# Kernel tuning notes

Measured on AMD Instinct MI355X. Metric: run time of the kernel, lower is better.

Reference implementation:

```python
import jax, jax.numpy as jnp
import numpy as np

N_NODES = 20000
N_EDGES = 320000
BERT_H = 768
GIN_H = 256
N_LAYERS = 3
EPS = 0.0  # gin_epsilon


def setup_inputs() -> dict:
    key = jax.random.key(0)
    ks = jax.random.split(key, 12)
    node_embed = jax.random.normal(ks[0], (N_NODES, BERT_H), dtype=jnp.float32)
    edge_weight = jax.random.uniform(ks[1], (N_EDGES,), dtype=jnp.float32)
    src = jax.random.randint(ks[2], (N_EDGES,), 0, N_NODES, dtype=jnp.int32)
    dst = jax.random.randint(ks[3], (N_EDGES,), 0, N_NODES, dtype=jnp.int32)
    s = 0.02
    W0 = jax.random.normal(ks[4], (BERT_H, GIN_H), dtype=jnp.float32) * s
    b0 = jnp.zeros((GIN_H,), dtype=jnp.float32)
    W1 = jax.random.normal(ks[5], (GIN_H, GIN_H), dtype=jnp.float32) * s
    b1 = jnp.zeros((GIN_H,), dtype=jnp.float32)
    W2 = jax.random.normal(ks[6], (GIN_H, GIN_H), dtype=jnp.float32) * s
    b2 = jnp.zeros((GIN_H,), dtype=jnp.float32)
    Wr = jax.random.normal(ks[7], (N_LAYERS * GIN_H, GIN_H), dtype=jnp.float32) * s
    br = jnp.zeros((GIN_H,), dtype=jnp.float32)
    return {"node_embed": node_embed, "edge_weight": edge_weight,
            "W0": W0, "b0": b0, "W1": W1, "b1": b1, "W2": W2, "b2": b2,
            "Wr": Wr, "br": br, "src": src, "dst": dst}


def _gin_layer(h, edge_weight, src, dst, W, b):
    # edge-weighted sum aggregation: agg_i = sum_{(j->i)} w_ji * h_j
    msgs = h[src] * edge_weight[:, None]          # [E, d]
    agg = jax.ops.segment_sum(msgs, dst, num_segments=N_NODES)  # [N, d]
    rst = (1.0 + EPS) * h + agg
    return jax.nn.relu(rst @ W + b)


def reference(node_embed, edge_weight, W0, b0, W1, b1, W2, b2, Wr, br, src, dst):
    params = [(W0, b0), (W1, b1), (W2, b2)]
    h = node_embed
    outs = []
    for (W, b) in params:
        h = _gin_layer(h, edge_weight, src, dst, W, b)
        outs.append(h)
    cat = jnp.concatenate(outs, axis=-1)          # [N, n_layers*gin_h]
    return jax.nn.relu(cat) @ Wr + br             # [N, gin_h]
```

## Files before the change

kernel.cpp:

```cpp
#include <hip/hip_runtime.h>

#define NN 20000
#define NE 320000
#define BH 768
#define GH 256

typedef __attribute__((ext_vector_type(8))) short short8;
typedef __attribute__((ext_vector_type(4))) float f32x4;

__device__ __forceinline__ ushort f2bf(float x) {
    union { float f; unsigned u; } v; v.f = x;
    unsigned r = (v.u + 0x7FFFu + ((v.u >> 16) & 1u)) >> 16;
    return (ushort)r;
}
__device__ __forceinline__ float bf2f(ushort h) {
    union { unsigned u; float f; } v; v.u = ((unsigned)h) << 16;
    return v.f;
}
__device__ __forceinline__ ushort f2h(float x) {
    union { _Float16 h; ushort u; } v; v.h = (_Float16)x; return v.u;
}
__device__ __forceinline__ float h2f(ushort u) {
    union { _Float16 h; ushort u; } v; v.u = u; return (float)v.h;
}

__device__ __forceinline__ void gload_lds16(const void* g, void* l) {
    __builtin_amdgcn_global_load_lds(
        (const __attribute__((address_space(1))) void*)g,
        (__attribute__((address_space(3))) void*)l, 16, 0, 0);
}


__global__ void k_count(const int* __restrict__ dst, int* __restrict__ cnt, int E) {
    int i = blockIdx.x * blockDim.x + threadIdx.x;
    if (i < E) atomicAdd(&cnt[dst[i]], 1);
}

__global__ __launch_bounds__(1024)
void k_scan(const int* __restrict__ cnt, int* __restrict__ off,
            int* __restrict__ fill, int n) {
    __shared__ int sbuf[1024];
    const int tid  = threadIdx.x;
    const int base = tid * 20;
    int local[20];
    int s = 0;
    #pragma unroll
    for (int i = 0; i < 20; ++i) {
        const int idx = base + i;
        int v = (idx < n) ? cnt[idx] : 0;
        local[i] = s;
        s += v;
    }
    sbuf[tid] = s;
    __syncthreads();
    int sum = s;
    for (int ofs = 1; ofs < 1024; ofs <<= 1) {
        int other = (tid >= ofs) ? sbuf[tid - ofs] : 0;
        __syncthreads();
        sum += other;
        sbuf[tid] = sum;
        __syncthreads();
    }
    const int excl = sum - s;
    #pragma unroll
    for (int i = 0; i < 20; ++i) {
        const int idx = base + i;
        if (idx < n) { const int v = excl + local[i]; off[idx] = v; fill[idx] = v; }
    }
    if (tid == 1023) off[n] = sum;
}

__global__ void k_scatter(const int* __restrict__ src, const int* __restrict__ dst,
                          const float* __restrict__ w, int* __restrict__ fill,
                          int* __restrict__ csr_src, float* __restrict__ csr_w, int E) {
    int i = blockIdx.x * blockDim.x + threadIdx.x;
    if (i < E) {
        int d = dst[i];
        int p = atomicAdd(&fill[d], 1);
        csr_src[p] = src[i];
        csr_w[p]  = w[i];
    }
}


__global__ void k_split(const float* __restrict__ x, ushort* __restrict__ hi,
                        ushort* __restrict__ lo, int n4) {
    int i = blockIdx.x * blockDim.x + threadIdx.x;
    if (i >= n4) return;
    float4 v = ((const float4*)x)[i];
    ushort4 h, l;
    h.x = f2bf(v.x); l.x = f2bf(v.x - bf2f(h.x));
    h.y = f2bf(v.y); l.y = f2bf(v.y - bf2f(h.y));
    h.z = f2bf(v.z); l.z = f2bf(v.z - bf2f(h.z));
    h.w = f2bf(v.w); l.w = f2bf(v.w - bf2f(h.w));
    ((ushort4*)hi)[i] = h;
    ((ushort4*)lo)[i] = l;
}

__global__ void k_splitw(const float* __restrict__ W, ushort* __restrict__ hi,
                         ushort* __restrict__ lo, int K, int N) {
    int id = blockIdx.x * blockDim.x + threadIdx.x;
    if (id >= K * N) return;
    int n = id / K, k = id % K;
    float v = W[(size_t)k * N + n];
    ushort h = f2bf(v);
    hi[id] = h;
    lo[id] = f2bf(v - bf2f(h));
}


__global__ __launch_bounds__(256)
void k_gemm_mfma(const ushort* __restrict__ Ah, const ushort* __restrict__ Al,
                 int lda, int K,
                 const ushort* __restrict__ Bh, const ushort* __restrict__ Bl,
                 const float* __restrict__ bias,
                 float* __restrict__ C, ushort* __restrict__ Ch, int M) {
    __shared__ ushort As_h[2][64 * 32];
    __shared__ ushort As_l[2][64 * 32];
    __shared__ ushort Bs_h[2][128 * 32];
    __shared__ ushort Bs_l[2][128 * 32];

    const int t    = threadIdx.x;
    const int lane = t & 63;
    const int m0   = blockIdx.y * 64;
    const int n0   = blockIdx.x * 128;

    const int ra = t >> 2;
    const int sa = (t & 3) ^ ((ra >> 1) & 3);
    int rga = m0 + ra; if (rga > M - 1) rga = M - 1;
    const size_t aofs = (size_t)rga * lda + (size_t)(sa * 8);
    const int cb1 = t + 256;
    const int rb0 = t >> 2,   rb1 = cb1 >> 2;
    const int sb0 = (t & 3)   ^ ((rb0 >> 1) & 3);
    const int sb1 = (cb1 & 3) ^ ((rb1 >> 1) & 3);
    const size_t bofs0 = (size_t)(n0 + rb0) * K + (size_t)(sb0 * 8);
    const size_t bofs1 = (size_t)(n0 + rb1) * K + (size_t)(sb1 * 8);
    const int d0 = (t >> 6) << 10;
    const int d1 = (cb1 >> 6) << 10;

    const int wm = (t >> 6) & 1;
    const int wn = t >> 7;

    f32x4 zero = (f32x4)0.0f;
    f32x4 acc[2][4];
    #pragma unroll
    for (int i = 0; i < 2; ++i)
        #pragma unroll
        for (int j = 0; j < 4; ++j) acc[i][j] = zero;

    const int fr  = lane & 15;
    const int fsl = lane >> 4;

    auto STAGE = [&](int buf, int k0) {
        gload_lds16(Ah + aofs + k0, (char*)As_h[buf] + d0);
        gload_lds16(Al + aofs + k0, (char*)As_l[buf] + d0);
        gload_lds16(Bh + bofs0 + k0, (char*)Bs_h[buf] + d0);
        gload_lds16(Bh + bofs1 + k0, (char*)Bs_h[buf] + d1);
        gload_lds16(Bl + bofs0 + k0, (char*)Bs_l[buf] + d0);
        gload_lds16(Bl + bofs1 + k0, (char*)Bs_l[buf] + d1);
    };

    STAGE(0, 0);
    int cur = 0;
    for (int k0 = 0; k0 < K; k0 += 32, cur ^= 1) {
        __syncthreads();
        if (k0 + 32 < K) STAGE(cur ^ 1, k0 + 32);

        short8 ah[2], al2[2], bh[4], bl[4];
        #pragma unroll
        for (int i = 0; i < 2; ++i) {
            const int r = wm * 32 + i * 16 + fr;
            const int s = fsl ^ ((r >> 1) & 3);
            ah[i]  = *(const short8*)(&As_h[cur][0] + r * 32 + s * 8);
            al2[i] = *(const short8*)(&As_l[cur][0] + r * 32 + s * 8);
        }
        #pragma unroll
        for (int j = 0; j < 4; ++j) {
            const int r = wn * 64 + j * 16 + fr;
            const int s = fsl ^ ((r >> 1) & 3);
            bh[j] = *(const short8*)(&Bs_h[cur][0] + r * 32 + s * 8);
            bl[j] = *(const short8*)(&Bs_l[cur][0] + r * 32 + s * 8);
        }
        #pragma unroll
        for (int i = 0; i < 2; ++i)
            #pragma unroll
            for (int j = 0; j < 4; ++j) {
                acc[i][j] = __builtin_amdgcn_mfma_f32_16x16x32_bf16(ah[i],  bh[j], acc[i][j], 0, 0, 0);
                acc[i][j] = __builtin_amdgcn_mfma_f32_16x16x32_bf16(ah[i],  bl[j], acc[i][j], 0, 0, 0);
                acc[i][j] = __builtin_amdgcn_mfma_f32_16x16x32_bf16(al2[i], bh[j], acc[i][j], 0, 0, 0);
            }
    }

    #pragma unroll
    for (int i = 0; i < 2; ++i) {
        #pragma unroll
        for (int j = 0; j < 4; ++j) {
            const int col = n0 + wn * 64 + j * 16 + fr;
            const int r0  = m0 + wm * 32 + i * 16 + ((lane >> 4) << 2);
            const float ba = bias ? bias[col] : 0.0f;
            #pragma unroll
            for (int q = 0; q < 4; ++q) {
                const int r = r0 + q;
                if (r < M) {
                    const float v = acc[i][j][q] + ba;
                    C[(size_t)r * 256 + col] = v;
                    if (Ch) Ch[(size_t)r * 256 + col] = f2h(v);
                }
            }
        }
    }
}


__global__ __launch_bounds__(256)
void k_aggregate(const float* __restrict__ y,
                 const ushort* __restrict__ yh,
                 const int* __restrict__ off,
                 const int* __restrict__ csr_src,
                 const float* __restrict__ csr_w,
                 const float* __restrict__ bias,
                 ushort* __restrict__ cat_h,
                 ushort* __restrict__ cat_l,
                 int n) {
    const int wave = blockIdx.x * (blockDim.x >> 6) + (threadIdx.x >> 6);
    const int lane = threadIdx.x & 63;
    if (wave >= n) return;
    const int c = lane * 4;

    float4 self = *(const float4*)(y + (size_t)wave * GH + c);
    float4 b    = *(const float4*)(bias + c);

    float4 a0 = make_float4(0.f, 0.f, 0.f, 0.f);
    float4 a1 = a0, a2 = a0, a3 = a0;
    const int e0 = off[wave], e1 = off[wave + 1];
    int e = e0;
    for (; e + 4 <= e1; e += 4) {
        const int   s0 = csr_src[e],     s1 = csr_src[e + 1];
        const int   s2 = csr_src[e + 2], s3 = csr_src[e + 3];
        const float w0 = csr_w[e],       w1 = csr_w[e + 1];
        const float w2 = csr_w[e + 2],   w3 = csr_w[e + 3];
        ushort4 v0 = *(const ushort4*)(yh + (size_t)s0 * GH + c);
        ushort4 v1 = *(const ushort4*)(yh + (size_t)s1 * GH + c);
        ushort4 v2 = *(const ushort4*)(yh + (size_t)s2 * GH + c);
        ushort4 v3 = *(const ushort4*)(yh + (size_t)s3 * GH + c);
        a0.x = fmaf(w0, h2f(v0.x), a0.x); a0.y = fmaf(w0, h2f(v0.y), a0.y);
        a0.z = fmaf(w0, h2f(v0.z), a0.z); a0.w = fmaf(w0, h2f(v0.w), a0.w);
        a1.x = fmaf(w1, h2f(v1.x), a1.x); a1.y = fmaf(w1, h2f(v1.y), a1.y);
        a1.z = fmaf(w1, h2f(v1.z), a1.z); a1.w = fmaf(w1, h2f(v1.w), a1.w);
        a2.x = fmaf(w2, h2f(v2.x), a2.x); a2.y = fmaf(w2, h2f(v2.y), a2.y);
        a2.z = fmaf(w2, h2f(v2.z), a2.z); a2.w = fmaf(w2, h2f(v2.w), a2.w);
        a3.x = fmaf(w3, h2f(v3.x), a3.x); a3.y = fmaf(w3, h2f(v3.y), a3.y);
        a3.z = fmaf(w3, h2f(v3.z), a3.z); a3.w = fmaf(w3, h2f(v3.w), a3.w);
    }
    for (; e < e1; ++e) {
        const int   s = csr_src[e];
        const float w = csr_w[e];
        ushort4 v = *(const ushort4*)(yh + (size_t)s * GH + c);
        a0.x = fmaf(w, h2f(v.x), a0.x); a0.y = fmaf(w, h2f(v.y), a0.y);
        a0.z = fmaf(w, h2f(v.z), a0.z); a0.w = fmaf(w, h2f(v.w), a0.w);
    }
    float4 r;
    r.x = fmaxf(self.x + ((a0.x + a1.x) + (a2.x + a3.x)) + b.x, 0.f);
    r.y = fmaxf(self.y + ((a0.y + a1.y) + (a2.y + a3.y)) + b.y, 0.f);
    r.z = fmaxf(self.z + ((a0.z + a1.z) + (a2.z + a3.z)) + b.z, 0.f);
    r.w = fmaxf(self.w + ((a0.w + a1.w) + (a2.w + a3.w)) + b.w, 0.f);
    ushort4 h, l;
    h.x = f2bf(r.x); l.x = f2bf(r.x - bf2f(h.x));
    h.y = f2bf(r.y); l.y = f2bf(r.y - bf2f(h.y));
    h.z = f2bf(r.z); l.z = f2bf(r.z - bf2f(h.z));
    h.w = f2bf(r.w); l.w = f2bf(r.w - bf2f(h.w));
    *(ushort4*)(cat_h + (size_t)wave * BH + c) = h;
    *(ushort4*)(cat_l + (size_t)wave * BH + c) = l;
}


extern "C" void kernel_launch(void* const* d_in, const int* in_sizes, int n_in,
                              void* d_out, int out_size, void* d_ws, size_t ws_size,
                              hipStream_t stream) {
    const float* node_embed = (const float*)d_in[0];
    const float* edge_w     = (const float*)d_in[1];
    const float* W0 = (const float*)d_in[2];
    const float* b0 = (const float*)d_in[3];
    const float* W1 = (const float*)d_in[4];
    const float* b1 = (const float*)d_in[5];
    const float* W2 = (const float*)d_in[6];
    const float* b2 = (const float*)d_in[7];
    const float* Wr = (const float*)d_in[8];
    const float* br = (const float*)d_in[9];
    const int* src  = (const int*)d_in[10];
    const int* dst  = (const int*)d_in[11];
    float* out = (float*)d_out;

    char* p = (char*)d_ws;
    auto carve = [&](size_t bytes) {
        void* r = (void*)p;
        p += (bytes + 255) & ~(size_t)255;
        return r;
    };
    ushort* plane_h = (ushort*)carve((size_t)NN * BH * 2);
    ushort* plane_l = (ushort*)carve((size_t)NN * BH * 2);
    float*  y       = (float*) carve((size_t)NN * GH * 4);
    ushort* yh      = (ushort*)carve((size_t)NN * GH * 2);
    ushort* wt0_h = (ushort*)carve((size_t)GH * BH * 2);
    ushort* wt0_l = (ushort*)carve((size_t)GH * BH * 2);
    ushort* wt1_h = (ushort*)carve((size_t)GH * GH * 2);
    ushort* wt1_l = (ushort*)carve((size_t)GH * GH * 2);
    ushort* wt2_h = (ushort*)carve((size_t)GH * GH * 2);
    ushort* wt2_l = (ushort*)carve((size_t)GH * GH * 2);
    ushort* wtr_h = (ushort*)carve((size_t)GH * BH * 2);
    ushort* wtr_l = (ushort*)carve((size_t)GH * BH * 2);
    int*    cnt     = (int*)  carve((size_t)NN * 4);
    int*    off     = (int*)  carve((size_t)(NN + 1) * 4);
    int*    fill    = (int*)  carve((size_t)NN * 4);
    int*    csr_src = (int*)  carve((size_t)NE * 4);
    float*  csr_w   = (float*)carve((size_t)NE * 4);
    (void)ws_size; (void)n_in; (void)in_sizes; (void)out_size;

    hipMemsetAsync(cnt, 0, (size_t)NN * 4, stream);
    k_count<<<(NE + 255) / 256, 256, 0, stream>>>(dst, cnt, NE);
    k_scan<<<1, 1024, 0, stream>>>(cnt, off, fill, NN);
    k_scatter<<<(NE + 255) / 256, 256, 0, stream>>>(src, dst, edge_w, fill,
                                                    csr_src, csr_w, NE);

    const int n4 = NN * BH / 4;
    k_split<<<(n4 + 255) / 256, 256, 0, stream>>>(node_embed, plane_h, plane_l, n4);
    k_splitw<<<(BH * GH + 255) / 256, 256, 0, stream>>>(W0, wt0_h, wt0_l, BH, GH);
    k_splitw<<<(GH * GH + 255) / 256, 256, 0, stream>>>(W1, wt1_h, wt1_l, GH, GH);
    k_splitw<<<(GH * GH + 255) / 256, 256, 0, stream>>>(W2, wt2_h, wt2_l, GH, GH);
    k_splitw<<<(BH * GH + 255) / 256, 256, 0, stream>>>(Wr, wtr_h, wtr_l, BH, GH);

    dim3 gemm_grid(2, (NN + 63) / 64);
    const int agg_blocks = (NN + 3) / 4;

    k_gemm_mfma<<<gemm_grid, 256, 0, stream>>>(plane_h, plane_l, BH, BH,
                                               wt0_h, wt0_l, nullptr, y, yh, NN);
    k_aggregate<<<agg_blocks, 256, 0, stream>>>(y, yh, off, csr_src, csr_w, b0,
                                                plane_h + 0, plane_l + 0, NN);
    k_gemm_mfma<<<gemm_grid, 256, 0, stream>>>(plane_h, plane_l, BH, GH,
                                               wt1_h, wt1_l, nullptr, y, yh, NN);
    k_aggregate<<<agg_blocks, 256, 0, stream>>>(y, yh, off, csr_src, csr_w, b1,
                                                plane_h + GH, plane_l + GH, NN);
    k_gemm_mfma<<<gemm_grid, 256, 0, stream>>>(plane_h + GH, plane_l + GH, BH, GH,
                                               wt2_h, wt2_l, nullptr, y, yh, NN);
    k_aggregate<<<agg_blocks, 256, 0, stream>>>(y, yh, off, csr_src, csr_w, b2,
                                                plane_h + 2 * GH, plane_l + 2 * GH, NN);
    k_gemm_mfma<<<gemm_grid, 256, 0, stream>>>(plane_h, plane_l, BH, BH,
                                               wtr_h, wtr_l, br, out, nullptr, NN);
}
```

Measured before the change: 403.7 us.

## Triple-buffer GEMM LDS pipeline and drop fp32 intermediate from aggregation

The GEMM moves from a double-buffered to a triple-buffered LDS pipeline. Explicit vmcnt waits let two async tile loads stay in flight while the current tile is computed. Separately, the per-layer GEMM no longer writes an fp32 copy of its output. The aggregation reads the self term from the fp16 copy it already gathers from, which removes an N×256 fp32 store and load per layer. The cost is more LDS per block, which may lower occupancy, and a self term rounded to fp16, which slightly reduces precision.

```diff
diff --git a/kernel.cpp b/kernel.cpp
--- a/kernel.cpp
+++ b/kernel.cpp
@@ -115,10 +115,10 @@
                  const ushort* __restrict__ Bh, const ushort* __restrict__ Bl,
                  const float* __restrict__ bias,
                  float* __restrict__ C, ushort* __restrict__ Ch, int M) {
-    __shared__ ushort As_h[2][64 * 32];
-    __shared__ ushort As_l[2][64 * 32];
-    __shared__ ushort Bs_h[2][128 * 32];
-    __shared__ ushort Bs_l[2][128 * 32];
+    __shared__ ushort As_h[3][64 * 32];
+    __shared__ ushort As_l[3][64 * 32];
+    __shared__ ushort Bs_h[3][128 * 32];
+    __shared__ ushort Bs_l[3][128 * 32];
 
     const int t    = threadIdx.x;
     const int lane = t & 63;
@@ -160,26 +160,36 @@
         gload_lds16(Bl + bofs1 + k0, (char*)Bs_l[buf] + d1);
     };
 
+    const int nt = K >> 5;
     STAGE(0, 0);
-    int cur = 0;
-    for (int k0 = 0; k0 < K; k0 += 32, cur ^= 1) {
-        __syncthreads();
-        if (k0 + 32 < K) STAGE(cur ^ 1, k0 + 32);
+    STAGE(1, 32);
+    for (int tt = 0; tt < nt; ++tt) {
+        if (tt < nt - 1) asm volatile("s_waitcnt vmcnt(6)" ::: "memory");
+        else             asm volatile("s_waitcnt vmcnt(0)" ::: "memory");
+        __builtin_amdgcn_s_barrier();
+        asm volatile("" ::: "memory");
+        if (tt + 2 < nt) STAGE((tt + 2) % 3, (tt + 2) << 5);
+
+        const int cur = tt % 3;
+        const ushort* ash = As_h[cur];
+        const ushort* asl = As_l[cur];
+        const ushort* bsh = Bs_h[cur];
+        const ushort* bsl = Bs_l[cur];
 
         short8 ah[2], al2[2], bh[4], bl[4];
         #pragma unroll
         for (int i = 0; i < 2; ++i) {
             const int r = wm * 32 + i * 16 + fr;
             const int s = fsl ^ ((r >> 1) & 3);
-            ah[i]  = *(const short8*)(&As_h[cur][0] + r * 32 + s * 8);
-            al2[i] = *(const short8*)(&As_l[cur][0] + r * 32 + s * 8);
+            ah[i]  = *(const short8*)(ash + r * 32 + s * 8);
+            al2[i] = *(const short8*)(asl + r * 32 + s * 8);
         }
         #pragma unroll
         for (int j = 0; j < 4; ++j) {
             const int r = wn * 64 + j * 16 + fr;
             const int s = fsl ^ ((r >> 1) & 3);
-            bh[j] = *(const short8*)(&Bs_h[cur][0] + r * 32 + s * 8);
-            bl[j] = *(const short8*)(&Bs_l[cur][0] + r * 32 + s * 8);
+            bh[j] = *(const short8*)(bsh + r * 32 + s * 8);
+            bl[j] = *(const short8*)(bsl + r * 32 + s * 8);
         }
         #pragma unroll
         for (int i = 0; i < 2; ++i)
@@ -203,7 +213,7 @@
                 const int r = r0 + q;
                 if (r < M) {
                     const float v = acc[i][j][q] + ba;
-                    C[(size_t)r * 256 + col] = v;
+                    if (C)  C[(size_t)r * 256 + col]  = v;
                     if (Ch) Ch[(size_t)r * 256 + col] = f2h(v);
                 }
             }
@@ -213,8 +223,7 @@
 
 
 __global__ __launch_bounds__(256)
-void k_aggregate(const float* __restrict__ y,
-                 const ushort* __restrict__ yh,
+void k_aggregate(const ushort* __restrict__ yh,
                  const int* __restrict__ off,
                  const int* __restrict__ csr_src,
                  const float* __restrict__ csr_w,
@@ -227,8 +236,8 @@
     if (wave >= n) return;
     const int c = lane * 4;
 
-    float4 self = *(const float4*)(y + (size_t)wave * GH + c);
-    float4 b    = *(const float4*)(bias + c);
+    ushort4 sh = *(const ushort4*)(yh + (size_t)wave * GH + c);
+    float4 b   = *(const float4*)(bias + c);
 
     float4 a0 = make_float4(0.f, 0.f, 0.f, 0.f);
     float4 a1 = a0, a2 = a0, a3 = a0;
@@ -260,10 +269,10 @@
         a0.z = fmaf(w, h2f(v.z), a0.z); a0.w = fmaf(w, h2f(v.w), a0.w);
     }
     float4 r;
-    r.x = fmaxf(self.x + ((a0.x + a1.x) + (a2.x + a3.x)) + b.x, 0.f);
-    r.y = fmaxf(self.y + ((a0.y + a1.y) + (a2.y + a3.y)) + b.y, 0.f);
-    r.z = fmaxf(self.z + ((a0.z + a1.z) + (a2.z + a3.z)) + b.z, 0.f);
-    r.w = fmaxf(self.w + ((a0.w + a1.w) + (a2.w + a3.w)) + b.w, 0.f);
+    r.x = fmaxf(h2f(sh.x) + ((a0.x + a1.x) + (a2.x + a3.x)) + b.x, 0.f);
+    r.y = fmaxf(h2f(sh.y) + ((a0.y + a1.y) + (a2.y + a3.y)) + b.y, 0.f);
+    r.z = fmaxf(h2f(sh.z) + ((a0.z + a1.z) + (a2.z + a3.z)) + b.z, 0.f);
+    r.w = fmaxf(h2f(sh.w) + ((a0.w + a1.w) + (a2.w + a3.w)) + b.w, 0.f);
     ushort4 h, l;
     h.x = f2bf(r.x); l.x = f2bf(r.x - bf2f(h.x));
     h.y = f2bf(r.y); l.y = f2bf(r.y - bf2f(h.y));
@@ -299,7 +308,6 @@
     };
     ushort* plane_h = (ushort*)carve((size_t)NN * BH * 2);
     ushort* plane_l = (ushort*)carve((size_t)NN * BH * 2);
-    float*  y       = (float*) carve((size_t)NN * GH * 4);
     ushort* yh      = (ushort*)carve((size_t)NN * GH * 2);
     ushort* wt0_h = (ushort*)carve((size_t)GH * BH * 2);
     ushort* wt0_l = (ushort*)carve((size_t)GH * BH * 2);
@@ -333,16 +341,16 @@
     const int agg_blocks = (NN + 3) / 4;
 
     k_gemm_mfma<<<gemm_grid, 256, 0, stream>>>(plane_h, plane_l, BH, BH,
-                                               wt0_h, wt0_l, nullptr, y, yh, NN);
-    k_aggregate<<<agg_blocks, 256, 0, stream>>>(y, yh, off, csr_src, csr_w, b0,
+                                               wt0_h, wt0_l, nullptr, nullptr, yh, NN);
+    k_aggregate<<<agg_blocks, 256, 0, stream>>>(yh, off, csr_src, csr_w, b0,
                                                 plane_h + 0, plane_l + 0, NN);
     k_gemm_mfma<<<gemm_grid, 256, 0, stream>>>(plane_h, plane_l, BH, GH,
-                                               wt1_h, wt1_l, nullptr, y, yh, NN);
-    k_aggregate<<<agg_blocks, 256, 0, stream>>>(y, yh, off, csr_src, csr_w, b1,
+                                               wt1_h, wt1_l, nullptr, nullptr, yh, NN);
+    k_aggregate<<<agg_blocks, 256, 0, stream>>>(yh, off, csr_src, csr_w, b1,
                                                 plane_h + GH, plane_l + GH, NN);
     k_gemm_mfma<<<gemm_grid, 256, 0, stream>>>(plane_h + GH, plane_l + GH, BH, GH,
-                                               wt2_h, wt2_l, nullptr, y, yh, NN);
-    k_aggregate<<<agg_blocks, 256, 0, stream>>>(y, yh, off, csr_src, csr_w, b2,
+                                               wt2_h, wt2_l, nullptr, nullptr, yh, NN);
+    k_aggregate<<<agg_blocks, 256, 0, stream>>>(yh, off, csr_src, csr_w, b2,
                                                 plane_h + 2 * GH, plane_l + 2 * GH, NN);
     k_gemm_mfma<<<gemm_grid, 256, 0, stream>>>(plane_h, plane_l, BH, BH,
                                                wtr_h, wtr_l, br, out, nullptr, NN);
```

Result: slower. 433.2 us (+7.3%).
